# Performance work log

Hardware: AMD Instinct MI355X
Metric: run time of the kernel (lower is better)

The kernel has to match this reference:

```python
import jax, jax.numpy as jnp
import numpy as np

PI = 3.14159  # matches the torch.jit.script gaussian constant


def _nonlinear(x, w1, b1, w2, b2):
    # Linear -> exact GELU -> Linear (torch F.gelu default is erf-based)
    return jax.nn.gelu(x @ w1 + b1, approximate=False) @ w2 + b2


def _gaussian_feature(dist, etype, mul_w, bias_w, means, stds):
    # dist: [..., R, C]; etype: [..., R, C] int
    mul = mul_w[etype]            # [..., R, C, 1]
    bias = bias_w[etype]          # [..., R, C, 1]
    x = mul * dist[..., None] + bias            # [..., R, C, 1]
    x = x - means                               # broadcast -> [..., R, C, K]
    std = jnp.abs(stds) + 1e-5                  # [K]
    a = (2.0 * PI) ** 0.5
    return jnp.exp(-0.5 * (x / std) ** 2) / (a * std)


def setup_inputs() -> dict:
    key = jax.random.key(0)
    ks = jax.random.split(key, 12)
    B, N, P, K, H, E = 2, 1024, 768, 128, 32, 1024
    pos = jax.random.normal(ks[0], (B, N, 3), dtype=jnp.float32)
    edge_types = jax.random.randint(ks[1], (B, N, N), 0, E)
    # GaussianLayer params (init per module)
    means = jax.random.uniform(ks[2], (K,), minval=0.0, maxval=3.0, dtype=jnp.float32)
    stds = jax.random.uniform(ks[3], (K,), minval=0.0, maxval=3.0, dtype=jnp.float32)
    mul_w = jnp.ones((E, 1), jnp.float32)
    bias_w = jnp.zeros((E, 1), jnp.float32)
    # out_proj: K -> K -> H
    ow1 = jax.random.normal(ks[4], (K, K), dtype=jnp.float32) * 0.05
    ob1 = jnp.zeros((K,), jnp.float32)
    ow2 = jax.random.normal(ks[5], (K, H), dtype=jnp.float32) * 0.05
    ob2 = jnp.zeros((H,), jnp.float32)
    # vector_proj: 3 -> 128 -> H
    vw1 = jax.random.normal(ks[6], (3, 128), dtype=jnp.float32) * 0.3
    vb1 = jnp.zeros((128,), jnp.float32)
    vw2 = jax.random.normal(ks[7], (128, H), dtype=jnp.float32) * 0.05
    vb2 = jnp.zeros((H,), jnp.float32)
    return {"pos": pos, "edge_types": edge_types, "protein_length": 768,
            "means": means, "stds": stds, "mul_w": mul_w, "bias_w": bias_w,
            "ow1": ow1, "ob1": ob1, "ow2": ow2, "ob2": ob2,
            "vw1": vw1, "vb1": vb1, "vw2": vw2, "vb2": vb2}


def reference(pos, edge_types, protein_length, means, stds, mul_w, bias_w,
              ow1, ob1, ow2, ob2, vw1, vb1, vw2, vb2):
    B, N, _ = pos.shape
    P = int(protein_length)
    L = N - P  # ligand nodes
    H = ow2.shape[1]

    lig = pos[:, :L]      # [B, L, 3]
    prot = pos[:, L:]     # [B, P, 3]

    dlm_ll = lig[:, None, :, :] - lig[:, :, None, :]    # [B, L, L, 3]
    dlm_lp = lig[:, None, :, :] - prot[:, :, None, :]   # [B, P, L, 3]
    dist_ll = 1.0 / (jnp.sum(dlm_ll ** 2, axis=-1) + 1.0)  # [B, L, L]
    dist_lp = 1.0 / (jnp.sum(dlm_lp ** 2, axis=-1) + 1.0)  # [B, P, L]

    dlm_ll_h = _nonlinear(dlm_ll, vw1, vb1, vw2, vb2)       # [B, L, L, H]
    dlm_pl_h = _nonlinear(-dlm_lp, vw1, vb1, vw2, vb2)      # [B, P, L, H]
    dlm_lp_h = _nonlinear(dlm_lp, vw1, vb1, vw2, vb2)       # [B, P, L, H]

    g_ll = _gaussian_feature(dist_ll, edge_types[:, :L, :L], mul_w, bias_w, means, stds)
    ef_ll = _nonlinear(g_ll, ow1, ob1, ow2, ob2)            # [B, L, L, H]
    g_lp = _gaussian_feature(dist_lp, edge_types[:, L:, :L], mul_w, bias_w, means, stds)
    ef_lp = _nonlinear(g_lp, ow1, ob1, ow2, ob2)            # [B, P, L, H]

    ef = jnp.zeros((B, N, N, H), jnp.float32)
    ef = ef.at[:, :L, :L, :].set(ef_ll + dlm_ll_h)
    ef = ef.at[:, L:, :L, :].set(ef_lp + dlm_lp_h)
    ef = ef.at[:, :L, L:, :].set(jnp.swapaxes(ef_lp + dlm_pl_h, 1, 2))

    return jnp.transpose(ef, (0, 3, 1, 2))  # [B, H, N, N]
```

## Files before the change

kernel.cpp:

```cpp
#include <hip/hip_runtime.h>
#include <math.h>


typedef __attribute__((__ext_vector_type__(8))) short bfrag;
typedef __attribute__((__ext_vector_type__(4))) float fx4;

#define MFMA_BF16(A, B, C) __builtin_amdgcn_mfma_f32_16x16x32_bf16((A), (B), (C), 0, 0, 0)

#define OFF_ISTD 0
#define OFF_MS   128
#define OFF_C2   256
#define OFF_BIAS 384
#define OFF_W3   416
#define OFF_FLAG 512
#define WS_H_BASE 1024
#define HOFF_OW1 0
#define HOFF_OW2 16384
#define HOFF_VW2 20480

#define N_MAIN 4096
#define N_PP   2304
#define PP_ITERS 16

__device__ __forceinline__ float rcp_f(float x) {
#if __has_builtin(__builtin_amdgcn_rcpf)
  return __builtin_amdgcn_rcpf(x);
#else
  return 1.0f / x;
#endif
}
__device__ __forceinline__ float exp2_f(float x) {
#if __has_builtin(__builtin_amdgcn_exp2f)
  return __builtin_amdgcn_exp2f(x);
#else
  return exp2f(x);
#endif
}
__device__ __forceinline__ unsigned short f2bf(float f) {
  unsigned u = __builtin_bit_cast(unsigned, f);
  return (unsigned short)((u + 0x7fffu + ((u >> 16) & 1u)) >> 16);
}
__device__ __forceinline__ float gelu_t(float x) {
  float z = x * x;
  float p = x * __builtin_fmaf(z, -0.10294324f, -2.30220821f);
  float e = exp2_f(p);
  return x * rcp_f(1.0f + e);
}

__global__ void setup_kernel(const float* __restrict__ means, const float* __restrict__ stds,
                             const float* __restrict__ ow1, const float* __restrict__ ow2,
                             const float* __restrict__ vw1, const float* __restrict__ vw2,
                             const float* __restrict__ ob2, const float* __restrict__ vb2,
                             const float* __restrict__ vb1, float* __restrict__ wsf) {
  int id = blockIdx.x * 256 + threadIdx.x;
  unsigned short* wsh = (unsigned short*)(wsf + WS_H_BASE);

  if (id < 128) {
    float s = fabsf(stds[id]) + 1e-5f;
    float inv = 1.0f / s;
    wsf[OFF_ISTD + id] = inv;
    wsf[OFF_MS + id] = means[id] * inv;
    wsf[OFF_C2 + id] = inv * 0.3989422804f;
  } else if (id < 160) {
    int h = id - 128;
    wsf[OFF_BIAS + h] = ob2[h] + vb2[h];
  } else if (id < 256) {
    int t = id - 160; int c = t >> 5, h = t & 31;
    float s = 0.0f;
    for (int k = 0; k < 128; ++k) s += vw1[c * 128 + k] * vw2[k * 32 + h];
    wsf[OFF_W3 + c * 32 + h] = s;
  } else if (id == 256) {
    int f = 1;
    for (int k = 0; k < 128; ++k) if (vb1[k] != 0.0f) f = 0;
    ((int*)wsf)[OFF_FLAG] = f;
  }
  for (int idx = id; idx < 16384; idx += 4096) {
    int k = idx >> 7, n = idx & 127;
    int pos = ((n >> 4) * 4 + (k >> 5)) * 512 + ((n & 15) * 4 + ((k >> 3) & 3)) * 8 + (k & 7);
    wsh[HOFF_OW1 + pos] = f2bf(ow1[idx]);
  }
  {
    int idx = id;
    int k = idx >> 5, n = idx & 31;
    int pos = ((n >> 4) * 4 + (k >> 5)) * 512 + ((n & 15) * 4 + ((k >> 3) & 3)) * 8 + (k & 7);
    wsh[HOFF_OW2 + pos] = f2bf(ow2[idx]);
    wsh[HOFF_VW2 + pos] = f2bf(vw2[idx]);
  }
}

__global__ __launch_bounds__(256, 2) void main_kernel(
    const float* __restrict__ pos, const int* __restrict__ etyp,
    const float* __restrict__ mulw, const float* __restrict__ biasw,
    const float* __restrict__ ob1, const float* __restrict__ vw1,
    const float* __restrict__ vb1, const float* __restrict__ wsf,
    float* __restrict__ out) {
  if (blockIdx.x >= N_MAIN) {
    int id = (blockIdx.x - N_MAIN) * 256 + threadIdx.x;
    fx4 z = {0.f, 0.f, 0.f, 0.f};
#pragma unroll
    for (int i = 0; i < PP_ITERS; ++i) {
      int idx = id + i * 589824;
      int c4 = idx % 192;
      int t2 = idx / 192;
      int r = t2 % 768;
      int bh = t2 / 768;
      *(fx4*)(out + (((long)bh) << 20) + ((long)(256 + r) << 10) + 256 + c4 * 4) = z;
    }
    return;
  }

  const unsigned short* wsh = (const unsigned short*)(wsf + WS_H_BASE);
  __shared__ unsigned short hef[4096];
  __shared__ unsigned short hlp[4096];
  __shared__ unsigned short hpl[4096];
  __shared__ float dlmb[512];
  __shared__ float outb[4224];

  int tid = threadIdx.x;
  int lane = tid & 63, w = tid >> 6;
  int q = lane >> 4, c15 = lane & 15;

  int t = blockIdx.x;
  int b, row0, col0;
  bool is_lp;
  if (t < 1024) {
    is_lp = false;
    b = t >> 9;
    int r = t & 511;
    row0 = (r >> 4) << 3;
    col0 = (r & 15) << 4;
  } else {
    is_lp = true;
    int t2 = t - 1024;
    b = t2 / 1536;
    int r = t2 % 1536;
    row0 = 256 + ((r >> 4) << 3);
    col0 = (r & 15) << 4;
  }
  int flag = ((const int*)wsf)[OFF_FLAG];

  bfrag gfr[2][4];
  float Ae[2];
  for (int mi = 0; mi < 2; ++mi) {
    int rloc = 2 * w + mi;
    int rowg = row0 + rloc, colg = col0 + c15;
    const float* pr = pos + ((b << 10) + rowg) * 3;
    const float* pc = pos + ((b << 10) + colg) * 3;
    float dx = pc[0] - pr[0], dy = pc[1] - pr[1], dz = pc[2] - pr[2];
    float d2 = __builtin_fmaf(dx, dx, __builtin_fmaf(dy, dy, dz * dz));
    float dist = rcp_f(d2 + 1.0f);
    int et = etyp[(b << 20) + (rowg << 10) + colg];
    Ae[mi] = __builtin_fmaf(mulw[et], dist, biasw[et]);
    if (q == 0) {
      int e = rloc * 16 + c15;
      dlmb[e * 4 + 0] = dx; dlmb[e * 4 + 1] = dy; dlmb[e * 4 + 2] = dz;
    }
  }
#pragma unroll
  for (int kc = 0; kc < 4; ++kc) {
    int k0 = kc * 32 + q * 8;
    fx4 is0 = *(const fx4*)(wsf + OFF_ISTD + k0);
    fx4 is1 = *(const fx4*)(wsf + OFF_ISTD + k0 + 4);
    fx4 ms0 = *(const fx4*)(wsf + OFF_MS + k0);
    fx4 ms1 = *(const fx4*)(wsf + OFF_MS + k0 + 4);
    fx4 cc0 = *(const fx4*)(wsf + OFF_C2 + k0);
    fx4 cc1 = *(const fx4*)(wsf + OFF_C2 + k0 + 4);
#pragma unroll
    for (int mi = 0; mi < 2; ++mi) {
      bfrag fr;
#pragma unroll
      for (int j = 0; j < 8; ++j) {
        float is = (j < 4) ? is0[j & 3] : is1[j & 3];
        float msv = (j < 4) ? ms0[j & 3] : ms1[j & 3];
        float ccv = (j < 4) ? cc0[j & 3] : cc1[j & 3];
        float y = __builtin_fmaf(Ae[mi], is, -msv);
        float g = exp2_f(y * y * (-0.72134752f)) * ccv;
        fr[j] = (short)f2bf(g);
      }
      gfr[mi][kc] = fr;
    }
  }
  __syncthreads();

  float ob1v[8];
#pragma unroll
  for (int i = 0; i < 8; ++i) ob1v[i] = ob1[i * 16 + c15];

  fx4 zero4 = {0.f, 0.f, 0.f, 0.f};
  fx4 aef[2][2], alp[2][2], apl[2][2];
#pragma unroll
  for (int mi = 0; mi < 2; ++mi)
#pragma unroll
    for (int nh = 0; nh < 2; ++nh) { aef[mi][nh] = zero4; alp[mi][nh] = zero4; apl[mi][nh] = zero4; }

  int oct = tid & 3, e0 = tid >> 2;

  for (int c2 = 0; c2 < 4; ++c2) {
    fx4 a1[2][2];
#pragma unroll
    for (int mi = 0; mi < 2; ++mi) { a1[mi][0] = zero4; a1[mi][1] = zero4; }
#pragma unroll
    for (int kc = 0; kc < 4; ++kc) {
      bfrag b0 = *(const bfrag*)(wsh + HOFF_OW1 + (((c2 * 2 + 0) * 4 + kc) * 512 + (c15 * 4 + q) * 8));
      bfrag b1 = *(const bfrag*)(wsh + HOFF_OW1 + (((c2 * 2 + 1) * 4 + kc) * 512 + (c15 * 4 + q) * 8));
      a1[0][0] = MFMA_BF16(gfr[0][kc], b0, a1[0][0]);
      a1[0][1] = MFMA_BF16(gfr[0][kc], b1, a1[0][1]);
      a1[1][0] = MFMA_BF16(gfr[1][kc], b0, a1[1][0]);
      a1[1][1] = MFMA_BF16(gfr[1][kc], b1, a1[1][1]);
    }
#pragma unroll
    for (int mi = 0; mi < 2; ++mi)
#pragma unroll
      for (int nt = 0; nt < 2; ++nt) {
        float bb = ob1v[c2 * 2 + nt];
#pragma unroll
        for (int r = 0; r < 4; ++r) {
          float v = gelu_t(a1[mi][nt][r] + bb);
          hef[(2 * w + mi) * 512 + ((q * 4 + r) * 4 + nt * 2 + ((lane >> 3) & 1)) * 8 + (lane & 7)] = f2bf(v);
        }
      }
    {
      int kk0 = c2 * 32 + oct * 8;
      fx4 w1a0 = *(const fx4*)(vw1 + kk0);
      fx4 w1a1 = *(const fx4*)(vw1 + kk0 + 4);
      fx4 w1b0 = *(const fx4*)(vw1 + 128 + kk0);
      fx4 w1b1 = *(const fx4*)(vw1 + 128 + kk0 + 4);
      fx4 w1c0 = *(const fx4*)(vw1 + 256 + kk0);
      fx4 w1c1 = *(const fx4*)(vw1 + 256 + kk0 + 4);
      fx4 vb0 = *(const fx4*)(vb1 + kk0);
      fx4 vb1q = *(const fx4*)(vb1 + kk0 + 4);
#pragma unroll
      for (int pass = 0; pass < 2; ++pass) {
        int e = e0 + (pass << 6);
        float dx = dlmb[e * 4 + 0], dy = dlmb[e * 4 + 1], dz = dlmb[e * 4 + 2];
        bfrag fl, fp;
#pragma unroll
        for (int j = 0; j < 8; ++j) {
          float wa = (j < 4) ? w1a0[j & 3] : w1a1[j & 3];
          float wb = (j < 4) ? w1b0[j & 3] : w1b1[j & 3];
          float wc = (j < 4) ? w1c0[j & 3] : w1c1[j & 3];
          float bb = (j < 4) ? vb0[j & 3] : vb1q[j & 3];
          float u0 = __builtin_fmaf(dx, wa, __builtin_fmaf(dy, wb, dz * wc));
          fl[j] = (short)f2bf(gelu_t(u0 + bb));
          if (!flag) fp[j] = (short)f2bf(gelu_t(bb - u0));
        }
        *((bfrag*)(hlp + (e >> 4) * 512 + ((e & 15) * 4 + oct) * 8)) = fl;
        if (!flag) *((bfrag*)(hpl + (e >> 4) * 512 + ((e & 15) * 4 + oct) * 8)) = fp;
      }
    }
    __syncthreads();
#pragma unroll
    for (int mi = 0; mi < 2; ++mi) {
      int mt = 2 * w + mi;
      bfrag a_ef = *(const bfrag*)(hef + mt * 512 + (c15 * 4 + q) * 8);
      bfrag a_lp = *(const bfrag*)(hlp + mt * 512 + (c15 * 4 + q) * 8);
#pragma unroll
      for (int nh = 0; nh < 2; ++nh) {
        bfrag b_o = *(const bfrag*)(wsh + HOFF_OW2 + ((nh * 4 + c2) * 512 + (c15 * 4 + q) * 8));
        bfrag b_v = *(const bfrag*)(wsh + HOFF_VW2 + ((nh * 4 + c2) * 512 + (c15 * 4 + q) * 8));
        aef[mi][nh] = MFMA_BF16(a_ef, b_o, aef[mi][nh]);
        alp[mi][nh] = MFMA_BF16(a_lp, b_v, alp[mi][nh]);
        if (!flag) {
          bfrag a_pl = *(const bfrag*)(hpl + mt * 512 + (c15 * 4 + q) * 8);
          apl[mi][nh] = MFMA_BF16(a_pl, b_v, apl[mi][nh]);
        }
      }
    }
    __syncthreads();
  }

  float bs0 = wsf[OFF_BIAS + c15];
  float bs1 = wsf[OFF_BIAS + 16 + c15];
#pragma unroll
  for (int mi = 0; mi < 2; ++mi) {
    int mt = 2 * w + mi;
#pragma unroll
    for (int nh = 0; nh < 2; ++nh) {
      float bb = nh ? bs1 : bs0;
      fx4 v;
#pragma unroll
      for (int r = 0; r < 4; ++r) v[r] = aef[mi][nh][r] + alp[mi][nh][r] + bb;
      *(fx4*)(outb + (nh * 16 + c15) * 132 + mt * 16 + q * 4) = v;
    }
  }
  __syncthreads();

  long base = (((long)(b * 32)) << 20) + (((long)row0) << 10) + col0;
#pragma unroll
  for (int i = 0; i < 4; ++i) {
    int it = tid + (i << 8);
    int h = it >> 5, rr = (it >> 2) & 7, c4v = it & 3;
    fx4 v = *(const fx4*)(outb + h * 132 + rr * 16 + c4v * 4);
    *(fx4*)(out + base + (((long)h) << 20) + (rr << 10) + c4v * 4) = v;
  }

  if (is_lp) {
    if (flag) {
#pragma unroll
      for (int i = 0; i < 4; ++i) {
        int it = tid + (i << 8);
        int h = it >> 5, rr2 = (it >> 1) & 15, p4 = it & 1;
        float w30 = wsf[OFF_W3 + h];
        float w31 = wsf[OFF_W3 + 32 + h];
        float w32 = wsf[OFF_W3 + 64 + h];
        fx4 v;
#pragma unroll
        for (int k = 0; k < 4; ++k) {
          int e = (p4 * 4 + k) * 16 + rr2;
          float val = outb[h * 132 + e];
          float dx = dlmb[e * 4 + 0], dy = dlmb[e * 4 + 1], dz = dlmb[e * 4 + 2];
          v[k] = val - __builtin_fmaf(dx, w30, __builtin_fmaf(dy, w31, dz * w32));
        }
        *(fx4*)(out + (((long)(b * 32 + h)) << 20) + (((long)(col0 + rr2)) << 10) + row0 + p4 * 4) = v;
      }
    } else {
      __syncthreads();
#pragma unroll
      for (int mi = 0; mi < 2; ++mi) {
        int mt = 2 * w + mi;
#pragma unroll
        for (int nh = 0; nh < 2; ++nh) {
          float bb = nh ? bs1 : bs0;
          fx4 v;
#pragma unroll
          for (int r = 0; r < 4; ++r) v[r] = aef[mi][nh][r] + apl[mi][nh][r] + bb;
          *(fx4*)(outb + (nh * 16 + c15) * 132 + mt * 16 + q * 4) = v;
        }
      }
      __syncthreads();
#pragma unroll
      for (int i = 0; i < 4; ++i) {
        int it = tid + (i << 8);
        int h = it >> 5, rr2 = (it >> 1) & 15, p4 = it & 1;
        fx4 v;
#pragma unroll
        for (int k = 0; k < 4; ++k) {
          int e = (p4 * 4 + k) * 16 + rr2;
          v[k] = outb[h * 132 + e];
        }
        *(fx4*)(out + (((long)(b * 32 + h)) << 20) + (((long)(col0 + rr2)) << 10) + row0 + p4 * 4) = v;
      }
    }
  }
}

extern "C" void kernel_launch(void* const* d_in, const int* in_sizes, int n_in,
                              void* d_out, int out_size, void* d_ws, size_t ws_size,
                              hipStream_t stream) {
  const float* pos   = (const float*)d_in[0];
  const int*   etyp  = (const int*)d_in[1];
  const float* means = (const float*)d_in[3];
  const float* stds  = (const float*)d_in[4];
  const float* mulw  = (const float*)d_in[5];
  const float* biasw = (const float*)d_in[6];
  const float* ow1   = (const float*)d_in[7];
  const float* ob1   = (const float*)d_in[8];
  const float* ow2   = (const float*)d_in[9];
  const float* ob2   = (const float*)d_in[10];
  const float* vw1   = (const float*)d_in[11];
  const float* vb1   = (const float*)d_in[12];
  const float* vw2   = (const float*)d_in[13];
  const float* vb2   = (const float*)d_in[14];
  float* out = (float*)d_out;
  float* wsf = (float*)d_ws;

  setup_kernel<<<dim3(16), dim3(256), 0, stream>>>(means, stds, ow1, ow2, vw1, vw2,
                                                   ob2, vb2, vb1, wsf);
  main_kernel<<<dim3(N_MAIN + N_PP), dim3(256), 0, stream>>>(pos, etyp, mulw, biasw,
                                                             ob1, vw1, vb1, wsf, out);
}
```

Baseline: 392.9 us.

## Split main kernel into specialized zero-bias fast path and general path

```diff
diff --git a/kernel.cpp b/kernel.cpp
--- a/kernel.cpp
+++ b/kernel.cpp
@@ -21,6 +21,7 @@
 #define N_MAIN 4096
 #define N_PP   2304
 #define PP_ITERS 16
+#define N_TOTAL (N_MAIN + N_PP)
 
 __device__ __forceinline__ float rcp_f(float x) {
 #if __has_builtin(__builtin_amdgcn_rcpf)
@@ -39,6 +40,10 @@
 __device__ __forceinline__ unsigned short f2bf(float f) {
   unsigned u = __builtin_bit_cast(unsigned, f);
   return (unsigned short)((u + 0x7fffu + ((u >> 16) & 1u)) >> 16);
+}
+__device__ __forceinline__ unsigned short f2bf_fast(float f) {
+  unsigned u = __builtin_bit_cast(unsigned, f);
+  return (unsigned short)((u + 0x8000u) >> 16);
 }
 __device__ __forceinline__ float gelu_t(float x) {
   float z = x * x;
@@ -88,26 +93,245 @@
   }
 }
 
-__global__ __launch_bounds__(256, 2) void main_kernel(
+__device__ __forceinline__ void decode_block(int bidx, bool& is_pp, int& sub) {
+  int g = bidx / 25, r = bidx % 25;
+  if (r >= 16) { is_pp = true;  sub = g * 9 + (r - 16); }
+  else         { is_pp = false; sub = g * 16 + r; }
+}
+
+__device__ __forceinline__ void pp_fill(int pp_id, float* __restrict__ out, int tid) {
+  int id = pp_id * 256 + tid;
+  fx4 z = {0.f, 0.f, 0.f, 0.f};
+#pragma unroll
+  for (int i = 0; i < PP_ITERS; ++i) {
+    int idx = id + i * 589824;
+    int c4 = idx % 192;
+    int t2 = idx / 192;
+    int r = t2 % 768;
+    int bh = t2 / 768;
+    *(fx4*)(out + (((long)bh) << 20) + ((long)(256 + r) << 10) + 256 + c4 * 4) = z;
+  }
+}
+
+__global__ __launch_bounds__(256, 4) void main_fast(
+    const float* __restrict__ pos, const int* __restrict__ etyp,
+    const float* __restrict__ mulw, const float* __restrict__ biasw,
+    const float* __restrict__ ob1, const float* __restrict__ vw1,
+    const float* __restrict__ wsf, float* __restrict__ out) {
+  int flag = ((const int*)wsf)[OFF_FLAG];
+  if (!flag) return;
+
+  int tid = threadIdx.x;
+  bool is_pp; int sub;
+  decode_block(blockIdx.x, is_pp, sub);
+  if (is_pp) { pp_fill(sub, out, tid); return; }
+
+  const unsigned short* wsh = (const unsigned short*)(wsf + WS_H_BASE);
+  __shared__ union {
+    struct { unsigned short hef[4096]; unsigned short hlp[4096]; } s;
+    float outb[4224];
+  } u;
+  __shared__ float dlmb[512];
+
+  int lane = tid & 63, w = tid >> 6;
+  int q = lane >> 4, c15 = lane & 15;
+
+  int t = sub;
+  int b, row0, col0;
+  bool is_lp;
+  if (t < 1024) {
+    is_lp = false;
+    b = t >> 9;
+    int r = t & 511;
+    row0 = (r >> 4) << 3;
+    col0 = (r & 15) << 4;
+  } else {
+    is_lp = true;
+    int t2 = t - 1024;
+    b = t2 / 1536;
+    int r = t2 % 1536;
+    row0 = 256 + ((r >> 4) << 3);
+    col0 = (r & 15) << 4;
+  }
+
+  bfrag gfr[2][4];
+  float Ae[2];
+  for (int mi = 0; mi < 2; ++mi) {
+    int rloc = 2 * w + mi;
+    int rowg = row0 + rloc, colg = col0 + c15;
+    const float* pr = pos + ((b << 10) + rowg) * 3;
+    const float* pc = pos + ((b << 10) + colg) * 3;
+    float dx = pc[0] - pr[0], dy = pc[1] - pr[1], dz = pc[2] - pr[2];
+    float d2 = __builtin_fmaf(dx, dx, __builtin_fmaf(dy, dy, dz * dz));
+    float dist = rcp_f(d2 + 1.0f);
+    int et = etyp[(b << 20) + (rowg << 10) + colg];
+    Ae[mi] = __builtin_fmaf(mulw[et], dist, biasw[et]);
+    if (q == 0) {
+      int e = rloc * 16 + c15;
+      dlmb[e * 4 + 0] = dx; dlmb[e * 4 + 1] = dy; dlmb[e * 4 + 2] = dz;
+    }
+  }
+#pragma unroll
+  for (int kc = 0; kc < 4; ++kc) {
+    int k0 = kc * 32 + q * 8;
+    fx4 is0 = *(const fx4*)(wsf + OFF_ISTD + k0);
+    fx4 is1 = *(const fx4*)(wsf + OFF_ISTD + k0 + 4);
+    fx4 ms0 = *(const fx4*)(wsf + OFF_MS + k0);
+    fx4 ms1 = *(const fx4*)(wsf + OFF_MS + k0 + 4);
+    fx4 cc0 = *(const fx4*)(wsf + OFF_C2 + k0);
+    fx4 cc1 = *(const fx4*)(wsf + OFF_C2 + k0 + 4);
+#pragma unroll
+    for (int mi = 0; mi < 2; ++mi) {
+      bfrag fr;
+#pragma unroll
+      for (int j = 0; j < 8; ++j) {
+        float is = (j < 4) ? is0[j & 3] : is1[j & 3];
+        float msv = (j < 4) ? ms0[j & 3] : ms1[j & 3];
+        float ccv = (j < 4) ? cc0[j & 3] : cc1[j & 3];
+        float y = __builtin_fmaf(Ae[mi], is, -msv);
+        float g = exp2_f(y * y * (-0.72134752f)) * ccv;
+        fr[j] = (short)f2bf_fast(g);
+      }
+      gfr[mi][kc] = fr;
+    }
+  }
+  __syncthreads();
+
+  float ob1v[8];
+#pragma unroll
+  for (int i = 0; i < 8; ++i) ob1v[i] = ob1[i * 16 + c15];
+
+  fx4 zero4 = {0.f, 0.f, 0.f, 0.f};
+  fx4 aef[2][2], alp[2][2];
+#pragma unroll
+  for (int mi = 0; mi < 2; ++mi)
+#pragma unroll
+    for (int nh = 0; nh < 2; ++nh) { aef[mi][nh] = zero4; alp[mi][nh] = zero4; }
+
+  int oct = tid & 3, e0 = tid >> 2;
+
+  for (int c2 = 0; c2 < 4; ++c2) {
+    fx4 a1[2][2];
+#pragma unroll
+    for (int mi = 0; mi < 2; ++mi) { a1[mi][0] = zero4; a1[mi][1] = zero4; }
+#pragma unroll
+    for (int kc = 0; kc < 4; ++kc) {
+      bfrag b0 = *(const bfrag*)(wsh + HOFF_OW1 + (((c2 * 2 + 0) * 4 + kc) * 512 + (c15 * 4 + q) * 8));
+      bfrag b1 = *(const bfrag*)(wsh + HOFF_OW1 + (((c2 * 2 + 1) * 4 + kc) * 512 + (c15 * 4 + q) * 8));
+      a1[0][0] = MFMA_BF16(gfr[0][kc], b0, a1[0][0]);
+      a1[0][1] = MFMA_BF16(gfr[0][kc], b1, a1[0][1]);
+      a1[1][0] = MFMA_BF16(gfr[1][kc], b0, a1[1][0]);
+      a1[1][1] = MFMA_BF16(gfr[1][kc], b1, a1[1][1]);
+    }
+#pragma unroll
+    for (int mi = 0; mi < 2; ++mi)
+#pragma unroll
+      for (int nt = 0; nt < 2; ++nt) {
+        float bb = ob1v[c2 * 2 + nt];
+#pragma unroll
+        for (int r = 0; r < 4; ++r) {
+          float v = gelu_t(a1[mi][nt][r] + bb);
+          u.s.hef[(2 * w + mi) * 512 + ((q * 4 + r) * 4 + nt * 2 + ((lane >> 3) & 1)) * 8 + (lane & 7)] = f2bf_fast(v);
+        }
+      }
+    {
+      int kk0 = c2 * 32 + oct * 8;
+      fx4 w1a0 = *(const fx4*)(vw1 + kk0);
+      fx4 w1a1 = *(const fx4*)(vw1 + kk0 + 4);
+      fx4 w1b0 = *(const fx4*)(vw1 + 128 + kk0);
+      fx4 w1b1 = *(const fx4*)(vw1 + 128 + kk0 + 4);
+      fx4 w1c0 = *(const fx4*)(vw1 + 256 + kk0);
+      fx4 w1c1 = *(const fx4*)(vw1 + 256 + kk0 + 4);
+#pragma unroll
+      for (int pass = 0; pass < 2; ++pass) {
+        int e = e0 + (pass << 6);
+        float dx = dlmb[e * 4 + 0], dy = dlmb[e * 4 + 1], dz = dlmb[e * 4 + 2];
+        bfrag fl;
+#pragma unroll
+        for (int j = 0; j < 8; ++j) {
+          float wa = (j < 4) ? w1a0[j & 3] : w1a1[j & 3];
+          float wb = (j < 4) ? w1b0[j & 3] : w1b1[j & 3];
+          float wc = (j < 4) ? w1c0[j & 3] : w1c1[j & 3];
+          float u0 = __builtin_fmaf(dx, wa, __builtin_fmaf(dy, wb, dz * wc));
+          fl[j] = (short)f2bf_fast(gelu_t(u0));
+        }
+        *((bfrag*)(u.s.hlp + (e >> 4) * 512 + ((e & 15) * 4 + oct) * 8)) = fl;
+      }
+    }
+    __syncthreads();
+#pragma unroll
+    for (int mi = 0; mi < 2; ++mi) {
+      int mt = 2 * w + mi;
+      bfrag a_ef = *(const bfrag*)(u.s.hef + mt * 512 + (c15 * 4 + q) * 8);
+      bfrag a_lp = *(const bfrag*)(u.s.hlp + mt * 512 + (c15 * 4 + q) * 8);
+#pragma unroll
+      for (int nh = 0; nh < 2; ++nh) {
+        bfrag b_o = *(const bfrag*)(wsh + HOFF_OW2 + ((nh * 4 + c2) * 512 + (c15 * 4 + q) * 8));
+        bfrag b_v = *(const bfrag*)(wsh + HOFF_VW2 + ((nh * 4 + c2) * 512 + (c15 * 4 + q) * 8));
+        aef[mi][nh] = MFMA_BF16(a_ef, b_o, aef[mi][nh]);
+        alp[mi][nh] = MFMA_BF16(a_lp, b_v, alp[mi][nh]);
+      }
+    }
+    __syncthreads();
+  }
+
+  float bs0 = wsf[OFF_BIAS + c15];
+  float bs1 = wsf[OFF_BIAS + 16 + c15];
+#pragma unroll
+  for (int mi = 0; mi < 2; ++mi) {
+    int mt = 2 * w + mi;
+#pragma unroll
+    for (int nh = 0; nh < 2; ++nh) {
+      float bb = nh ? bs1 : bs0;
+      fx4 v;
+#pragma unroll
+      for (int r = 0; r < 4; ++r) v[r] = aef[mi][nh][r] + alp[mi][nh][r] + bb;
+      *(fx4*)(u.outb + (nh * 16 + c15) * 132 + mt * 16 + q * 4) = v;
+    }
+  }
+  __syncthreads();
+
+  long base = (((long)(b * 32)) << 20) + (((long)row0) << 10) + col0;
+#pragma unroll
+  for (int i = 0; i < 4; ++i) {
+    int it = tid + (i << 8);
+    int h = it >> 5, rr = (it >> 2) & 7, c4v = it & 3;
+    fx4 v = *(const fx4*)(u.outb + h * 132 + rr * 16 + c4v * 4);
+    *(fx4*)(out + base + (((long)h) << 20) + (rr << 10) + c4v * 4) = v;
+  }
+
+  if (is_lp) {
+#pragma unroll
+    for (int i = 0; i < 4; ++i) {
+      int it = tid + (i << 8);
+      int h = it >> 5, rr2 = (it >> 1) & 15, p4 = it & 1;
+      float w30 = wsf[OFF_W3 + h];
+      float w31 = wsf[OFF_W3 + 32 + h];
+      float w32 = wsf[OFF_W3 + 64 + h];
+      fx4 v;
+#pragma unroll
+      for (int k = 0; k < 4; ++k) {
+        int e = (p4 * 4 + k) * 16 + rr2;
+        float val = u.outb[h * 132 + e];
+        float dx = dlmb[e * 4 + 0], dy = dlmb[e * 4 + 1], dz = dlmb[e * 4 + 2];
+        v[k] = val - __builtin_fmaf(dx, w30, __builtin_fmaf(dy, w31, dz * w32));
+      }
+      *(fx4*)(out + (((long)(b * 32 + h)) << 20) + (((long)(col0 + rr2)) << 10) + row0 + p4 * 4) = v;
+    }
+  }
+}
+
+__global__ __launch_bounds__(256, 2) void main_general(
     const float* __restrict__ pos, const int* __restrict__ etyp,
     const float* __restrict__ mulw, const float* __restrict__ biasw,
     const float* __restrict__ ob1, const float* __restrict__ vw1,
     const float* __restrict__ vb1, const float* __restrict__ wsf,
     float* __restrict__ out) {
-  if (blockIdx.x >= N_MAIN) {
-    int id = (blockIdx.x - N_MAIN) * 256 + threadIdx.x;
-    fx4 z = {0.f, 0.f, 0.f, 0.f};
-#pragma unroll
-    for (int i = 0; i < PP_ITERS; ++i) {
-      int idx = id + i * 589824;
-      int c4 = idx % 192;
-      int t2 = idx / 192;
-      int r = t2 % 768;
-      int bh = t2 / 768;
-      *(fx4*)(out + (((long)bh) << 20) + ((long)(256 + r) << 10) + 256 + c4 * 4) = z;
-    }
-    return;
-  }
+  int flag = ((const int*)wsf)[OFF_FLAG];
+  if (flag) return;
+
+  int tid = threadIdx.x;
+  if (blockIdx.x >= N_MAIN) { pp_fill(blockIdx.x - N_MAIN, out, tid); return; }
 
   const unsigned short* wsh = (const unsigned short*)(wsf + WS_H_BASE);
   __shared__ unsigned short hef[4096];
@@ -116,7 +340,6 @@
   __shared__ float dlmb[512];
   __shared__ float outb[4224];
 
-  int tid = threadIdx.x;
   int lane = tid & 63, w = tid >> 6;
   int q = lane >> 4, c15 = lane & 15;
 
@@ -137,7 +360,6 @@
     row0 = 256 + ((r >> 4) << 3);
     col0 = (r & 15) << 4;
   }
-  int flag = ((const int*)wsf)[OFF_FLAG];
 
   bfrag gfr[2][4];
   float Ae[2];
@@ -242,10 +464,10 @@
           float bb = (j < 4) ? vb0[j & 3] : vb1q[j & 3];
           float u0 = __builtin_fmaf(dx, wa, __builtin_fmaf(dy, wb, dz * wc));
           fl[j] = (short)f2bf(gelu_t(u0 + bb));
-          if (!flag) fp[j] = (short)f2bf(gelu_t(bb - u0));
+          fp[j] = (short)f2bf(gelu_t(bb - u0));
         }
         *((bfrag*)(hlp + (e >> 4) * 512 + ((e & 15) * 4 + oct) * 8)) = fl;
-        if (!flag) *((bfrag*)(hpl + (e >> 4) * 512 + ((e & 15) * 4 + oct) * 8)) = fp;
+        *((bfrag*)(hpl + (e >> 4) * 512 + ((e & 15) * 4 + oct) * 8)) = fp;
       }
     }
     __syncthreads();
@@ -254,16 +476,14 @@
       int mt = 2 * w + mi;
       bfrag a_ef = *(const bfrag*)(hef + mt * 512 + (c15 * 4 + q) * 8);
       bfrag a_lp = *(const bfrag*)(hlp + mt * 512 + (c15 * 4 + q) * 8);
+      bfrag a_pl = *(const bfrag*)(hpl + mt * 512 + (c15 * 4 + q) * 8);
 #pragma unroll
       for (int nh = 0; nh < 2; ++nh) {
         bfrag b_o = *(const bfrag*)(wsh + HOFF_OW2 + ((nh * 4 + c2) * 512 + (c15 * 4 + q) * 8));
         bfrag b_v = *(const bfrag*)(wsh + HOFF_VW2 + ((nh * 4 + c2) * 512 + (c15 * 4 + q) * 8));
         aef[mi][nh] = MFMA_BF16(a_ef, b_o, aef[mi][nh]);
         alp[mi][nh] = MFMA_BF16(a_lp, b_v, alp[mi][nh]);
-        if (!flag) {
-          bfrag a_pl = *(const bfrag*)(hpl + mt * 512 + (c15 * 4 + q) * 8);
-          apl[mi][nh] = MFMA_BF16(a_pl, b_v, apl[mi][nh]);
-        }
+        apl[mi][nh] = MFMA_BF16(a_pl, b_v, apl[mi][nh]);
       }
     }
     __syncthreads();
@@ -295,51 +515,31 @@
   }
 
   if (is_lp) {
-    if (flag) {
-#pragma unroll
-      for (int i = 0; i < 4; ++i) {
-        int it = tid + (i << 8);
-        int h = it >> 5, rr2 = (it >> 1) & 15, p4 = it & 1;
-        float w30 = wsf[OFF_W3 + h];
-        float w31 = wsf[OFF_W3 + 32 + h];
-        float w32 = wsf[OFF_W3 + 64 + h];
+    __syncthreads();
+#pragma unroll
+    for (int mi = 0; mi < 2; ++mi) {
+      int mt = 2 * w + mi;
+#pragma unroll
+      for (int nh = 0; nh < 2; ++nh) {
+        float bb = nh ? bs1 : bs0;
         fx4 v;
 #pragma unroll
-        for (int k = 0; k < 4; ++k) {
-          int e = (p4 * 4 + k) * 16 + rr2;
-          float val = outb[h * 132 + e];
-          float dx = dlmb[e * 4 + 0], dy = dlmb[e * 4 + 1], dz = dlmb[e * 4 + 2];
-          v[k] = val - __builtin_fmaf(dx, w30, __builtin_fmaf(dy, w31, dz * w32));
-        }
-        *(fx4*)(out + (((long)(b * 32 + h)) << 20) + (((long)(col0 + rr2)) << 10) + row0 + p4 * 4) = v;
-      }
-    } else {
-      __syncthreads();
-#pragma unroll
-      for (int mi = 0; mi < 2; ++mi) {
-        int mt = 2 * w + mi;
-#pragma unroll
-        for (int nh = 0; nh < 2; ++nh) {
-          float bb = nh ? bs1 : bs0;
-          fx4 v;
-#pragma unroll
-          for (int r = 0; r < 4; ++r) v[r] = aef[mi][nh][r] + apl[mi][nh][r] + bb;
-          *(fx4*)(outb + (nh * 16 + c15) * 132 + mt * 16 + q * 4) = v;
-        }
-      }
-      __syncthreads();
-#pragma unroll
-      for (int i = 0; i < 4; ++i) {
-        int it = tid + (i << 8);
-        int h = it >> 5, rr2 = (it >> 1) & 15, p4 = it & 1;
-        fx4 v;
-#pragma unroll
-        for (int k = 0; k < 4; ++k) {
-          int e = (p4 * 4 + k) * 16 + rr2;
-          v[k] = outb[h * 132 + e];
-        }
-        *(fx4*)(out + (((long)(b * 32 + h)) << 20) + (((long)(col0 + rr2)) << 10) + row0 + p4 * 4) = v;
-      }
+        for (int r = 0; r < 4; ++r) v[r] = aef[mi][nh][r] + apl[mi][nh][r] + bb;
+        *(fx4*)(outb + (nh * 16 + c15) * 132 + mt * 16 + q * 4) = v;
+      }
+    }
+    __syncthreads();
+#pragma unroll
+    for (int i = 0; i < 4; ++i) {
+      int it = tid + (i << 8);
+      int h = it >> 5, rr2 = (it >> 1) & 15, p4 = it & 1;
+      fx4 v;
+#pragma unroll
+      for (int k = 0; k < 4; ++k) {
+        int e = (p4 * 4 + k) * 16 + rr2;
+        v[k] = outb[h * 132 + e];
+      }
+      *(fx4*)(out + (((long)(b * 32 + h)) << 20) + (((long)(col0 + rr2)) << 10) + row0 + p4 * 4) = v;
     }
   }
 }
@@ -366,6 +566,8 @@
 
   setup_kernel<<<dim3(16), dim3(256), 0, stream>>>(means, stds, ow1, ow2, vw1, vw2,
                                                    ob2, vb2, vb1, wsf);
-  main_kernel<<<dim3(N_MAIN + N_PP), dim3(256), 0, stream>>>(pos, etyp, mulw, biasw,
-                                                             ob1, vw1, vb1, wsf, out);
-}
+  main_fast<<<dim3(N_TOTAL), dim3(256), 0, stream>>>(pos, etyp, mulw, biasw,
+                                                     ob1, vw1, wsf, out);
+  main_general<<<dim3(N_TOTAL), dim3(256), 0, stream>>>(pos, etyp, mulw, biasw,
+                                                        ob1, vw1, vb1, wsf, out);
+}
```

Result: slower. 410.5 us (+4.5%).
